# Optimization experiments

Hardware: AMD Instinct MI355X
Metric: run time of the kernel (lower is better)

## Reference

```python
import jax, jax.numpy as jnp
import numpy as np

NBODY = 63          # body 0 = world, body 1 = free-joint root, bodies 2..62 = hinge
NHINGE = NBODY - 2  # 61 hinge dofs -> qpos dim = 7 + 61 = 68
NSITES = 16
B = 131072


def _qmul(q1, q2):
    """Hamilton product, (w,x,y,z) convention. Broadcasts over leading dims."""
    w1, x1, y1, z1 = q1[..., 0], q1[..., 1], q1[..., 2], q1[..., 3]
    w2, x2, y2, z2 = q2[..., 0], q2[..., 1], q2[..., 2], q2[..., 3]
    return jnp.stack([
        w1 * w2 - x1 * x2 - y1 * y2 - z1 * z2,
        w1 * x2 + x1 * w2 + y1 * z2 - z1 * y2,
        w1 * y2 - x1 * z2 + y1 * w2 + z1 * x2,
        w1 * z2 + x1 * y2 - y1 * x2 + z1 * w2,
    ], axis=-1)


def _qrot(q, v):
    """Rotate v by unit quaternion q (equivalent to q*v*q^-1 sandwich)."""
    u = q[..., 1:]
    w = q[..., :1]
    t = 2.0 * jnp.cross(u, v)
    return v + w * t + jnp.cross(u, t)


def setup_inputs() -> dict:
    key = jax.random.key(0)
    ks = jax.random.split(key, 8)
    qpos = jax.random.normal(ks[0], (B, 7 + NHINGE), dtype=jnp.float32) * 0.3
    body_pos = jax.random.normal(ks[1], (NBODY, 3), dtype=jnp.float32) * 0.1
    bq = jax.random.normal(ks[2], (NBODY, 4), dtype=jnp.float32)
    body_quat = bq / jnp.linalg.norm(bq, axis=-1, keepdims=True)
    ax = jax.random.normal(ks[3], (NHINGE, 3), dtype=jnp.float32)
    hinge_axis = ax / jnp.linalg.norm(ax, axis=-1, keepdims=True)
    jnt_pos = jax.random.normal(ks[4], (NHINGE, 3), dtype=jnp.float32) * 0.05
    site_pos = jax.random.normal(ks[5], (NSITES, 3), dtype=jnp.float32) * 0.05
    body_parent = jnp.maximum(jnp.arange(NBODY, dtype=jnp.int32) - 1, 0)  # chain tree
    site_body = jax.random.randint(ks[6], (NSITES,), 1, NBODY, dtype=jnp.int32)
    return {
        'qpos': qpos, 'body_pos': body_pos, 'body_quat': body_quat,
        'hinge_axis': hinge_axis, 'jnt_pos': jnt_pos, 'site_pos': site_pos,
        'body_parent': body_parent, 'site_body': site_body,
    }


def reference(qpos, body_pos, body_quat, hinge_axis, jnt_pos, site_pos,
              body_parent, site_body):
    # Structural ints are static tree topology: pull to host for Python indexing.
    parents = np.asarray(body_parent)
    sbody = np.asarray(site_body)
    Bn = qpos.shape[0]
    nbody = body_pos.shape[0]

    wp = [None] * nbody  # per-body world position [B,3]
    wq = [None] * nbody  # per-body world quaternion [B,4]
    wp[0] = jnp.zeros((Bn, 3), dtype=qpos.dtype)
    wq[0] = jnp.broadcast_to(jnp.array([1.0, 0.0, 0.0, 0.0], dtype=qpos.dtype), (Bn, 4))

    # body 1: free joint -> root pos + normalized quat straight from qpos
    wp[1] = qpos[:, 0:3]
    q = qpos[:, 3:7]
    wq[1] = q / jnp.linalg.norm(q, axis=-1, keepdims=True)

    # hinge bodies, parents always processed before children
    for bid in range(2, nbody):
        h = bid - 2
        p = int(parents[bid])
        half = 0.5 * qpos[:, 7 + h]
        s, c = jnp.sin(half), jnp.cos(half)
        ax = hinge_axis[h]
        hq = jnp.stack([c, s * ax[0], s * ax[1], s * ax[2]], axis=-1)  # [B,4]
        local_combined = _qmul(jnp.broadcast_to(body_quat[bid], (Bn, 4)), hq)
        anchor = wp[p] + _qrot(wq[p], body_pos[bid] + jnt_pos[h])  # world joint anchor
        nq = _qmul(wq[p], local_combined)
        wq[bid] = nq
        wp[bid] = anchor - _qrot(nq, jnt_pos[h])

    WP = jnp.stack(wp, axis=1)  # [B, nbody, 3]
    WQ = jnp.stack(wq, axis=1)  # [B, nbody, 4]

    # sites: vectorized gather + rotate over all keypoint sites at once
    sq = WQ[:, sbody]                         # [B, S, 4]
    sp = WP[:, sbody]                         # [B, S, 3]
    sites = sp + _qrot(sq, site_pos[None, :, :])  # [B, S, 3]
    return sites
```

## Files before the change

### kernel.cpp

```cpp
#include <hip/hip_runtime.h>


#define NBODY  63
#define NHINGE 61
#define NSITES 16
#define QDIM   68
#define HROW   20

typedef unsigned long long u64;

__global__ __launch_bounds__(256, 2)
void fk_main(const float* __restrict__ qpos,
             const float* __restrict__ body_pos,
             const float* __restrict__ body_quat,
             const float* __restrict__ hinge_axis,
             const float* __restrict__ jnt_pos,
             const float* __restrict__ site_pos,
             const int* __restrict__ site_body,
             float* __restrict__ out, int nenv)
{
    __shared__ __align__(16) float hc[NHINGE * HROW];
    __shared__ float spos[NSITES][4];

    const int tid = threadIdx.x;
    const int t   = blockIdx.x * 256 + tid;

    if (tid < NHINGE) {
        int h = tid, bid = h + 2;
        float uw = body_quat[bid*4+0], ux = body_quat[bid*4+1];
        float uy = body_quat[bid*4+2], uz = body_quat[bid*4+3];
        float ax = hinge_axis[h*3+0], ay = hinge_axis[h*3+1], az = hinge_axis[h*3+2];
        float jx = jnt_pos[h*3+0],   jy = jnt_pos[h*3+1],   jz = jnt_pos[h*3+2];
        float bx = body_pos[bid*3+0], by = body_pos[bid*3+1], bz = body_pos[bid*3+2];
        auto qr = [&](float vx, float vy, float vz, float& ox, float& oy, float& oz) {
            float tx = 2.f*(uy*vz - uz*vy);
            float ty = 2.f*(uz*vx - ux*vz);
            float tz = 2.f*(ux*vy - uy*vx);
            ox = vx + uw*tx + (uy*tz - uz*ty);
            oy = vy + uw*ty + (uz*tx - ux*tz);
            oz = vz + uw*tz + (ux*ty - uy*tx);
        };
        float adj = ax*jx + ay*jy + az*jz;
        float dx = adj*ax, dy = adj*ay, dz = adj*az;
        float cxx = ay*jz - az*jy;
        float cxy = az*jx - ax*jz;
        float cxz = ax*jy - ay*jx;
        float r1x,r1y,r1z, r2x,r2y,r2z, r3x,r3y,r3z;
        qr(dx, dy, dz, r1x, r1y, r1z);
        qr(jx-dx, jy-dy, jz-dz, r2x, r2y, r2z);
        qr(cxx, cxy, cxz, r3x, r3y, r3z);
        float* o = hc + h * HROW;
        o[0] = uw; o[1] = ux; o[2] = uy; o[3] = uz;
        o[4] = -(ux*ax + uy*ay + uz*az);
        o[5] =  uw*ax + uy*az - uz*ay;
        o[6] =  uw*ay - ux*az + uz*ax;
        o[7] =  uw*az + ux*ay - uy*ax;
        o[8]  = bx + jx - r1x; o[9]  = by + jy - r1y; o[10] = bz + jz - r1z; o[11] = 0.f;
        o[12] = -r2x; o[13] = -r2y; o[14] = -r2z; o[15] = 0.f;
        o[16] = -r3x; o[17] = -r3y; o[18] = -r3z; o[19] = 0.f;
    }
    if (tid < NSITES) {
        spos[tid][0] = site_pos[tid*3+0];
        spos[tid][1] = site_pos[tid*3+1];
        spos[tid][2] = site_pos[tid*3+2];
        spos[tid][3] = 0.f;
    }

    int sbody[NSITES];
#pragma unroll
    for (int s = 0; s < NSITES; s++) sbody[s] = site_body[s];
    u64 bodymask = 0ull;
#pragma unroll
    for (int s = 0; s < NSITES; s++) bodymask |= 1ull << sbody[s];

    __syncthreads();

    if (t < nenv) {
        const float4* q4 = reinterpret_cast<const float4*>(qpos) + (size_t)t * 17;
        float4 c0 = q4[0], c1 = q4[1];
        float4 cur = q4[2];

        float wpx = c0.x, wpy = c0.y, wpz = c0.z;
        float qw = c0.w, qx = c1.x, qy = c1.y, qz = c1.z;
        float inv = rsqrtf(qw*qw + qx*qx + qy*qy + qz*qz);
        qw *= inv; qx *= inv; qy *= inv; qz *= inv;

        float o[48];

        auto emitBody = [&](int bid) {
#pragma unroll
            for (int s = 0; s < NSITES; s++) {
                if (sbody[s] == bid) {
                    float vx = spos[s][0], vy = spos[s][1], vz = spos[s][2];
                    float tx = 2.f*(qy*vz - qz*vy);
                    float ty = 2.f*(qz*vx - qx*vz);
                    float tz = 2.f*(qx*vy - qy*vx);
                    o[3*s+0] = wpx + vx + qw*tx + (qy*tz - qz*ty);
                    o[3*s+1] = wpy + vy + qw*ty + (qz*tx - qx*tz);
                    o[3*s+2] = wpz + vz + qw*tz + (qx*ty - qy*tx);
                }
            }
        };

        auto step = [&](int h, float ang) {
            const float* c = hc + h * HROW;
            float x = 0.5f * ang, x2 = x * x;
            float ps = __builtin_fmaf(8.3333333e-3f, x2, -1.6666667e-1f);
            ps = __builtin_fmaf(ps, x2, 1.f);
            float sn = ps * x;
            float pc = __builtin_fmaf(-1.3888889e-3f, x2, 4.1666668e-2f);
            pc = __builtin_fmaf(pc, x2, -0.5f);
            float cs = __builtin_fmaf(pc, x2, 1.f);
            float cosT = __builtin_fmaf(-2.f*sn, sn, 1.f);
            float sinT = (sn + sn) * cs;
            float lw = cs*c[0] + sn*c[4];
            float lx = cs*c[1] + sn*c[5];
            float ly = cs*c[2] + sn*c[6];
            float lz = cs*c[3] + sn*c[7];
            float tlx = c[8]  + c[12]*cosT + c[16]*sinT;
            float tly = c[9]  + c[13]*cosT + c[17]*sinT;
            float tlz = c[10] + c[14]*cosT + c[18]*sinT;
            float tx = 2.f*(qy*tlz - qz*tly);
            float ty = 2.f*(qz*tlx - qx*tlz);
            float tz = 2.f*(qx*tly - qy*tlx);
            wpx += tlx + qw*tx + (qy*tz - qz*ty);
            wpy += tly + qw*ty + (qz*tx - qx*tz);
            wpz += tlz + qw*tz + (qx*ty - qy*tx);
            float nw = qw*lw - qx*lx - qy*ly - qz*lz;
            float nx = qw*lx + qx*lw + qy*lz - qz*ly;
            float ny = qw*ly - qx*lz + qy*lw + qz*lx;
            float nz = qw*lz + qx*ly - qy*lx + qz*lw;
            qw = nw; qx = nx; qy = ny; qz = nz;
        };

        if (bodymask & 2ull) emitBody(1);
        step(0, c1.w);
        if (bodymask & 4ull) emitBody(2);

#pragma clang loop unroll(disable)
        for (int g = 0; g < 15; ++g) {
            float4 nxt = q4[g < 14 ? g + 3 : 16];
            int hb = 1 + 4 * g;
            step(hb,     cur.x);
            if ((bodymask >> (hb + 2)) & 1ull) emitBody(hb + 2);
            step(hb + 1, cur.y);
            if ((bodymask >> (hb + 3)) & 1ull) emitBody(hb + 3);
            step(hb + 2, cur.z);
            if ((bodymask >> (hb + 4)) & 1ull) emitBody(hb + 4);
            step(hb + 3, cur.w);
            if ((bodymask >> (hb + 5)) & 1ull) emitBody(hb + 5);
            cur = nxt;
        }

        float4* o4 = reinterpret_cast<float4*>(out + (size_t)t * 48);
#pragma unroll
        for (int i = 0; i < 12; i++) {
            float4 v = { o[4*i+0], o[4*i+1], o[4*i+2], o[4*i+3] };
            o4[i] = v;
        }
    }
}

extern "C" void kernel_launch(void* const* d_in, const int* in_sizes, int n_in,
                              void* d_out, int out_size, void* d_ws, size_t ws_size,
                              hipStream_t stream)
{
    const float* qpos       = (const float*)d_in[0];
    const float* body_pos   = (const float*)d_in[1];
    const float* body_quat  = (const float*)d_in[2];
    const float* hinge_axis = (const float*)d_in[3];
    const float* jnt_pos    = (const float*)d_in[4];
    const float* site_pos   = (const float*)d_in[5];
    const int* site_body    = (const int*)d_in[7];

    int nenv = in_sizes[0] / QDIM;

    fk_main<<<(nenv + 255) / 256, 256, 0, stream>>>(qpos, body_pos, body_quat,
                                                    hinge_axis, jnt_pos, site_pos,
                                                    site_body, (float*)d_out, nenv);
}
```

Baseline: 118.1 us.

## Split kinematic chain across four waves per env and compose segment transforms

Each environment's 61-hinge chain is now split into four segments handled by four wavefronts. Each wave computes its local transform and emits site positions relative to its segment start. A composition pass through shared memory then prefixes those site positions with the transforms of the earlier segments. Per-hinge constants and site masks move into a separate setup kernel that writes a workspace, and output is staged in shared memory for coalesced float4 stores. This shortens the serial dependency chain and raises parallelism, at the cost of extra syncs, an extra launch, sites emitted through runtime masks, and global (not LDS) constant reads.

Result: slower. 120.9 us (+2.4%).

```diff
diff --git a/kernel.cpp b/kernel.cpp
--- a/kernel.cpp
+++ b/kernel.cpp
@@ -4,106 +4,134 @@
 #define NBODY  63
 #define NHINGE 61
 #define NSITES 16
-#define QDIM   68
-#define HROW   20
-
-typedef unsigned long long u64;
-
-__global__ __launch_bounds__(256, 2)
-void fk_main(const float* __restrict__ qpos,
-             const float* __restrict__ body_pos,
-             const float* __restrict__ body_quat,
-             const float* __restrict__ hinge_axis,
-             const float* __restrict__ jnt_pos,
-             const float* __restrict__ site_pos,
-             const int* __restrict__ site_body,
+#define QDIM    68
+#define HROW    20
+#define EPB     64
+#define LSTRIDE 49
+
+#define HC_OFF  0
+#define SP_OFF  (64 * HROW)
+#define SM_OFF  (SP_OFF + 64)
+#define FEM_OFF (SM_OFF + 64)
+
+typedef unsigned int u32;
+
+__global__ void fk_setup(const float* __restrict__ body_pos, const float* __restrict__ body_quat,
+                         const float* __restrict__ hinge_axis, const float* __restrict__ jnt_pos,
+                         const float* __restrict__ site_pos, const int* __restrict__ site_body,
+                         float* __restrict__ ws)
+{
+    int tid = threadIdx.x;
+    if (tid < 64) {
+        float* o = ws + HC_OFF + tid * HROW;
+        if (tid < NHINGE) {
+            int h = tid, bid = h + 2;
+            float uw = body_quat[bid*4+0], ux = body_quat[bid*4+1];
+            float uy = body_quat[bid*4+2], uz = body_quat[bid*4+3];
+            float ax = hinge_axis[h*3+0], ay = hinge_axis[h*3+1], az = hinge_axis[h*3+2];
+            float jx = jnt_pos[h*3+0],   jy = jnt_pos[h*3+1],   jz = jnt_pos[h*3+2];
+            float bx = body_pos[bid*3+0], by = body_pos[bid*3+1], bz = body_pos[bid*3+2];
+            auto qr = [&](float vx, float vy, float vz, float& ox, float& oy, float& oz) {
+                float tx = 2.f*(uy*vz - uz*vy);
+                float ty = 2.f*(uz*vx - ux*vz);
+                float tz = 2.f*(ux*vy - uy*vx);
+                ox = vx + uw*tx + (uy*tz - uz*ty);
+                oy = vy + uw*ty + (uz*tx - ux*tz);
+                oz = vz + uw*tz + (ux*ty - uy*tx);
+            };
+            float adj = ax*jx + ay*jy + az*jz;
+            float dx = adj*ax, dy = adj*ay, dz = adj*az;
+            float cxx = ay*jz - az*jy;
+            float cxy = az*jx - ax*jz;
+            float cxz = ax*jy - ay*jx;
+            float r1x,r1y,r1z, r2x,r2y,r2z, r3x,r3y,r3z;
+            qr(dx, dy, dz, r1x, r1y, r1z);
+            qr(jx-dx, jy-dy, jz-dz, r2x, r2y, r2z);
+            qr(cxx, cxy, cxz, r3x, r3y, r3z);
+            o[0] = uw; o[1] = ux; o[2] = uy; o[3] = uz;
+            o[4] = -(ux*ax + uy*ay + uz*az);
+            o[5] =  uw*ax + uy*az - uz*ay;
+            o[6] =  uw*ay - ux*az + uz*ax;
+            o[7] =  uw*az + ux*ay - uy*ax;
+            o[8]  = bx + jx - r1x; o[9]  = by + jy - r1y; o[10] = bz + jz - r1z; o[11] = 0.f;
+            o[12] = -r2x; o[13] = -r2y; o[14] = -r2z; o[15] = 0.f;
+            o[16] = -r3x; o[17] = -r3y; o[18] = -r3z; o[19] = 0.f;
+        } else {
+            for (int i = 0; i < HROW; i++) o[i] = 0.f;
+        }
+    }
+    if (tid < NSITES) {
+        float* o = ws + SP_OFF + tid * 4;
+        o[0] = site_pos[tid*3+0];
+        o[1] = site_pos[tid*3+1];
+        o[2] = site_pos[tid*3+2];
+        o[3] = 0.f;
+    }
+    if (tid == 0) {
+        int* im = (int*)(ws + SM_OFF);
+        for (int b = 0; b < 64; b++) {
+            int m = 0;
+            if (b < NBODY)
+                for (int s = 0; s < NSITES; s++)
+                    if (site_body[s] == b) m |= 1 << s;
+            im[b] = m;
+        }
+        int* fe = (int*)(ws + FEM_OFF);
+        int f1 = 0, f2 = 0, f3 = 0;
+        for (int b = 18; b <= 33; b++) f1 |= im[b];
+        for (int b = 34; b <= 49; b++) f2 |= im[b];
+        for (int b = 50; b <= 62; b++) f3 |= im[b];
+        fe[0] = 0; fe[1] = f1; fe[2] = f2; fe[3] = f3;
+    }
+}
+
+__global__ __launch_bounds__(256)
+void fk_main(const float* __restrict__ qpos, const float* __restrict__ ws,
              float* __restrict__ out, int nenv)
 {
-    __shared__ __align__(16) float hc[NHINGE * HROW];
-    __shared__ float spos[NSITES][4];
+    __shared__ float sbuf[EPB * LSTRIDE];
+    __shared__ float sx[4][EPB][9];
 
     const int tid = threadIdx.x;
-    const int t   = blockIdx.x * 256 + tid;
-
-    if (tid < NHINGE) {
-        int h = tid, bid = h + 2;
-        float uw = body_quat[bid*4+0], ux = body_quat[bid*4+1];
-        float uy = body_quat[bid*4+2], uz = body_quat[bid*4+3];
-        float ax = hinge_axis[h*3+0], ay = hinge_axis[h*3+1], az = hinge_axis[h*3+2];
-        float jx = jnt_pos[h*3+0],   jy = jnt_pos[h*3+1],   jz = jnt_pos[h*3+2];
-        float bx = body_pos[bid*3+0], by = body_pos[bid*3+1], bz = body_pos[bid*3+2];
-        auto qr = [&](float vx, float vy, float vz, float& ox, float& oy, float& oz) {
-            float tx = 2.f*(uy*vz - uz*vy);
-            float ty = 2.f*(uz*vx - ux*vz);
-            float tz = 2.f*(ux*vy - uy*vx);
-            ox = vx + uw*tx + (uy*tz - uz*ty);
-            oy = vy + uw*ty + (uz*tx - ux*tz);
-            oz = vz + uw*tz + (ux*ty - uy*tx);
-        };
-        float adj = ax*jx + ay*jy + az*jz;
-        float dx = adj*ax, dy = adj*ay, dz = adj*az;
-        float cxx = ay*jz - az*jy;
-        float cxy = az*jx - ax*jz;
-        float cxz = ax*jy - ay*jx;
-        float r1x,r1y,r1z, r2x,r2y,r2z, r3x,r3y,r3z;
-        qr(dx, dy, dz, r1x, r1y, r1z);
-        qr(jx-dx, jy-dy, jz-dz, r2x, r2y, r2z);
-        qr(cxx, cxy, cxz, r3x, r3y, r3z);
-        float* o = hc + h * HROW;
-        o[0] = uw; o[1] = ux; o[2] = uy; o[3] = uz;
-        o[4] = -(ux*ax + uy*ay + uz*az);
-        o[5] =  uw*ax + uy*az - uz*ay;
-        o[6] =  uw*ay - ux*az + uz*ax;
-        o[7] =  uw*az + ux*ay - uy*ax;
-        o[8]  = bx + jx - r1x; o[9]  = by + jy - r1y; o[10] = bz + jz - r1z; o[11] = 0.f;
-        o[12] = -r2x; o[13] = -r2y; o[14] = -r2z; o[15] = 0.f;
-        o[16] = -r3x; o[17] = -r3y; o[18] = -r3z; o[19] = 0.f;
-    }
-    if (tid < NSITES) {
-        spos[tid][0] = site_pos[tid*3+0];
-        spos[tid][1] = site_pos[tid*3+1];
-        spos[tid][2] = site_pos[tid*3+2];
-        spos[tid][3] = 0.f;
-    }
-
-    int sbody[NSITES];
-#pragma unroll
-    for (int s = 0; s < NSITES; s++) sbody[s] = site_body[s];
-    u64 bodymask = 0ull;
-#pragma unroll
-    for (int s = 0; s < NSITES; s++) bodymask |= 1ull << sbody[s];
-
-    __syncthreads();
-
-    if (t < nenv) {
-        const float4* q4 = reinterpret_cast<const float4*>(qpos) + (size_t)t * 17;
-        float4 c0 = q4[0], c1 = q4[1];
-        float4 cur = q4[2];
-
-        float wpx = c0.x, wpy = c0.y, wpz = c0.z;
-        float qw = c0.w, qx = c1.x, qy = c1.y, qz = c1.z;
-        float inv = rsqrtf(qw*qw + qx*qx + qy*qy + qz*qz);
-        qw *= inv; qx *= inv; qy *= inv; qz *= inv;
-
-        float o[48];
-
-        auto emitBody = [&](int bid) {
-#pragma unroll
-            for (int s = 0; s < NSITES; s++) {
-                if (sbody[s] == bid) {
-                    float vx = spos[s][0], vy = spos[s][1], vz = spos[s][2];
-                    float tx = 2.f*(qy*vz - qz*vy);
-                    float ty = 2.f*(qz*vx - qx*vz);
-                    float tz = 2.f*(qx*vy - qy*vx);
-                    o[3*s+0] = wpx + vx + qw*tx + (qy*tz - qz*ty);
-                    o[3*s+1] = wpy + vy + qw*ty + (qz*tx - qx*tz);
-                    o[3*s+2] = wpz + vz + qw*tz + (qx*ty - qy*tx);
-                }
+    const int w   = __builtin_amdgcn_readfirstlane(tid >> 6);
+    const int l   = tid & 63;
+    const int env = blockIdx.x * EPB + l;
+    const bool active = (env < nenv);
+    float* my = sbuf + l * LSTRIDE;
+
+    const int*   smaskp = (const int*)(ws + SM_OFF);
+    const float* sposp  = ws + SP_OFF;
+
+    float ww = 1.f, wx = 0.f, wy = 0.f, wz = 0.f, px = 0.f, py = 0.f, pz = 0.f;
+
+    const int cb = 1 + 4 * w;
+
+    if (active) {
+        const float4* q4 = reinterpret_cast<const float4*>(qpos + (size_t)env * QDIM);
+        float4 c0 = q4[cb];
+        float4 cur = q4[cb + 1];
+
+        if (w == 0) {
+            float4 r0 = q4[0], r1 = q4[1];
+            float nw = r0.w, nx = r1.x, ny = r1.y, nz = r1.z;
+            float inv = rsqrtf(nw*nw + nx*nx + ny*ny + nz*nz);
+            ww = nw*inv; wx = nx*inv; wy = ny*inv; wz = nz*inv;
+            px = r0.x; py = r0.y; pz = r0.z;
+            int msk = smaskp[1];
+            while (msk) {
+                int s = __ffs(msk) - 1; msk &= msk - 1;
+                float vx = sposp[s*4+0], vy = sposp[s*4+1], vz = sposp[s*4+2];
+                float tx = 2.f*(wy*vz - wz*vy);
+                float ty = 2.f*(wz*vx - wx*vz);
+                float tz = 2.f*(wx*vy - wy*vx);
+                my[s*3+0] = px + vx + ww*tx + (wy*tz - wz*ty);
+                my[s*3+1] = py + vy + ww*ty + (wz*tx - wx*tz);
+                my[s*3+2] = pz + vz + ww*tz + (wx*ty - wy*tx);
             }
-        };
-
-        auto step = [&](int h, float ang) {
-            const float* c = hc + h * HROW;
+        }
+
+        auto step = [&](int m, float ang) {
+            const float* c = ws + HC_OFF + (16*w + m) * HROW;
             float x = 0.5f * ang, x2 = x * x;
             float ps = __builtin_fmaf(8.3333333e-3f, x2, -1.6666667e-1f);
             ps = __builtin_fmaf(ps, x2, 1.f);
@@ -120,43 +148,106 @@
             float tlx = c[8]  + c[12]*cosT + c[16]*sinT;
             float tly = c[9]  + c[13]*cosT + c[17]*sinT;
             float tlz = c[10] + c[14]*cosT + c[18]*sinT;
-            float tx = 2.f*(qy*tlz - qz*tly);
-            float ty = 2.f*(qz*tlx - qx*tlz);
-            float tz = 2.f*(qx*tly - qy*tlx);
-            wpx += tlx + qw*tx + (qy*tz - qz*ty);
-            wpy += tly + qw*ty + (qz*tx - qx*tz);
-            wpz += tlz + qw*tz + (qx*ty - qy*tx);
-            float nw = qw*lw - qx*lx - qy*ly - qz*lz;
-            float nx = qw*lx + qx*lw + qy*lz - qz*ly;
-            float ny = qw*ly - qx*lz + qy*lw + qz*lx;
-            float nz = qw*lz + qx*ly - qy*lx + qz*lw;
-            qw = nw; qx = nx; qy = ny; qz = nz;
+            float tx = 2.f*(wy*tlz - wz*tly);
+            float ty = 2.f*(wz*tlx - wx*tlz);
+            float tz = 2.f*(wx*tly - wy*tlx);
+            px += tlx + ww*tx + (wy*tz - wz*ty);
+            py += tly + ww*ty + (wz*tx - wx*tz);
+            pz += tlz + ww*tz + (wx*ty - wy*tx);
+            float nw = ww*lw - wx*lx - wy*ly - wz*lz;
+            float nx = ww*lx + wx*lw + wy*lz - wz*ly;
+            float ny = ww*ly - wx*lz + wy*lw + wz*lx;
+            float nz = ww*lz + wx*ly - wy*lx + wz*lw;
+            ww = nw; wx = nx; wy = ny; wz = nz;
         };
-
-        if (bodymask & 2ull) emitBody(1);
-        step(0, c1.w);
-        if (bodymask & 4ull) emitBody(2);
-
+        auto emitStep = [&](int m) {
+            int msk = smaskp[16*w + m + 2];
+            while (msk) {
+                int s = __ffs(msk) - 1; msk &= msk - 1;
+                float vx = sposp[s*4+0], vy = sposp[s*4+1], vz = sposp[s*4+2];
+                float tx = 2.f*(wy*vz - wz*vy);
+                float ty = 2.f*(wz*vx - wx*vz);
+                float tz = 2.f*(wx*vy - wy*vx);
+                my[s*3+0] = px + vx + ww*tx + (wy*tz - wz*ty);
+                my[s*3+1] = py + vy + ww*ty + (wz*tx - wx*tz);
+                my[s*3+2] = pz + vz + ww*tz + (wx*ty - wy*tx);
+            }
+        };
+
+        step(0, c0.w); emitStep(0);
 #pragma clang loop unroll(disable)
-        for (int g = 0; g < 15; ++g) {
-            float4 nxt = q4[g < 14 ? g + 3 : 16];
-            int hb = 1 + 4 * g;
-            step(hb,     cur.x);
-            if ((bodymask >> (hb + 2)) & 1ull) emitBody(hb + 2);
-            step(hb + 1, cur.y);
-            if ((bodymask >> (hb + 3)) & 1ull) emitBody(hb + 3);
-            step(hb + 2, cur.z);
-            if ((bodymask >> (hb + 4)) & 1ull) emitBody(hb + 4);
-            step(hb + 3, cur.w);
-            if ((bodymask >> (hb + 5)) & 1ull) emitBody(hb + 5);
+        for (int g = 0; g < 3; ++g) {
+            int ci = cb + 2 + g; ci = ci > 16 ? 16 : ci;
+            float4 nxt = q4[ci];
+            int mb = 1 + 4 * g;
+            step(mb,     cur.x); emitStep(mb);
+            step(mb + 1, cur.y); emitStep(mb + 1);
+            step(mb + 2, cur.z); emitStep(mb + 2);
+            step(mb + 3, cur.w); emitStep(mb + 3);
             cur = nxt;
         }
-
-        float4* o4 = reinterpret_cast<float4*>(out + (size_t)t * 48);
+        if (w < 3) {
+            step(13, cur.x); emitStep(13);
+            step(14, cur.y); emitStep(14);
+            step(15, cur.z); emitStep(15);
+        }
+
+        float* sxp = &sx[w][l][0];
+        sxp[0] = ww; sxp[1] = wx; sxp[2] = wy; sxp[3] = wz;
+        sxp[4] = px; sxp[5] = py; sxp[6] = pz;
+    }
+
+    __syncthreads();
+
+    if (w > 0 && active) {
+        float tw = sx[0][l][0], tx_ = sx[0][l][1], ty_ = sx[0][l][2], tz_ = sx[0][l][3];
+        float tpx = sx[0][l][4], tpy = sx[0][l][5], tpz = sx[0][l][6];
+        for (int j = 1; j < w; ++j) {
+            float aw = sx[j][l][0], ax = sx[j][l][1], ay = sx[j][l][2], az = sx[j][l][3];
+            float apx = sx[j][l][4], apy = sx[j][l][5], apz = sx[j][l][6];
+            float cx = 2.f*(ty_*apz - tz_*apy);
+            float cy = 2.f*(tz_*apx - tx_*apz);
+            float cz = 2.f*(tx_*apy - ty_*apx);
+            float npx = tpx + apx + tw*cx + (ty_*cz - tz_*cy);
+            float npy = tpy + apy + tw*cy + (tz_*cx - tx_*cz);
+            float npz = tpz + apz + tw*cz + (tx_*cy - ty_*cx);
+            float nw = tw*aw - tx_*ax - ty_*ay - tz_*az;
+            float nx = tw*ax + tx_*aw + ty_*az - tz_*ay;
+            float ny = tw*ay - tx_*az + ty_*aw + tz_*ax;
+            float nz = tw*az + tx_*ay - ty_*ax + tz_*aw;
+            tw = nw; tx_ = nx; ty_ = ny; tz_ = nz;
+            tpx = npx; tpy = npy; tpz = npz;
+        }
+        int fm = ((const int*)(ws + FEM_OFF))[w];
+        while (fm) {
+            int s = __ffs(fm) - 1; fm &= fm - 1;
+            float lx = my[s*3+0], ly = my[s*3+1], lz = my[s*3+2];
+            float cx = 2.f*(ty_*lz - tz_*ly);
+            float cy = 2.f*(tz_*lx - tx_*lz);
+            float cz = 2.f*(tx_*ly - ty_*lx);
+            my[s*3+0] = tpx + lx + tw*cx + (ty_*cz - tz_*cy);
+            my[s*3+1] = tpy + ly + tw*cy + (tz_*cx - tx_*cz);
+            my[s*3+2] = tpz + lz + tw*cz + (tx_*cy - ty_*cx);
+        }
+    }
+
+    __syncthreads();
+
+    {
+        size_t blk_f = (size_t)blockIdx.x * (EPB * 48);
+        if (blk_f + EPB * 48 <= (size_t)nenv * 48) {
+            float4* out4 = reinterpret_cast<float4*>(out + blk_f);
 #pragma unroll
-        for (int i = 0; i < 12; i++) {
-            float4 v = { o[4*i+0], o[4*i+1], o[4*i+2], o[4*i+3] };
-            o4[i] = v;
+            for (int kk = 0; kk < 3; kk++) {
+                int g = kk * 256 + tid;
+                int q = g / 12;
+                int r = (g - q * 12) * 4;
+                const float* p = sbuf + q * LSTRIDE + r;
+                float4 v = { p[0], p[1], p[2], p[3] };
+                out4[g] = v;
+            }
+        } else if (active && w == 0) {
+            for (int i = 0; i < 48; i++) out[(size_t)env * 48 + i] = my[i];
         }
     }
 }
@@ -172,10 +263,11 @@
     const float* jnt_pos    = (const float*)d_in[4];
     const float* site_pos   = (const float*)d_in[5];
     const int* site_body    = (const int*)d_in[7];
+    float* ws = (float*)d_ws;
 
     int nenv = in_sizes[0] / QDIM;
 
-    fk_main<<<(nenv + 255) / 256, 256, 0, stream>>>(qpos, body_pos, body_quat,
-                                                    hinge_axis, jnt_pos, site_pos,
-                                                    site_body, (float*)d_out, nenv);
+    fk_setup<<<1, 64, 0, stream>>>(body_pos, body_quat, hinge_axis, jnt_pos,
+                                   site_pos, site_body, ws);
+    fk_main<<<(nenv + EPB - 1) / EPB, 256, 0, stream>>>(qpos, ws, (float*)d_out, nenv);
 }
```
